# Optimization experiments

Hardware: AMD Instinct MI355X
Metric: run time of the kernel (lower is better)

The kernel has to match this reference:

```python
import jax, jax.numpy as jnp
import numpy as np

B, T, D_IN = 2048, 26, 512
H = 512          # hidden_size
E = 256          # num_char_embeddings
C = 97           # num_class
S = 32           # num_steps = batch_max_length + 1


def setup_inputs() -> dict:
    key = jax.random.key(0)
    ks = jax.random.split(key, 16)
    sc = lambda n: 1.0 / np.sqrt(n)
    inp = {
        "batch_H": jax.random.normal(ks[0], (B, T, D_IN), jnp.float32),
        "text": jax.random.randint(ks[1], (B, S), 0, C),
        # attention cell params
        "W_i2h": jax.random.normal(ks[2], (H, D_IN), jnp.float32) * sc(D_IN),
        "W_h2h": jax.random.normal(ks[3], (H, H), jnp.float32) * sc(H),
        "b_h2h": jax.random.normal(ks[4], (H,), jnp.float32) * sc(H),
        "w_score": jax.random.normal(ks[5], (1, H), jnp.float32) * sc(H),
        # LSTMCell params (gate order: i, f, g, o)
        "W_ih": jax.random.normal(ks[6], (4 * H, D_IN + E), jnp.float32) * sc(D_IN + E),
        "W_hh": jax.random.normal(ks[7], (4 * H, H), jnp.float32) * sc(H),
        "b_ih": jax.random.normal(ks[8], (4 * H,), jnp.float32) * sc(H),
        "b_hh": jax.random.normal(ks[9], (4 * H,), jnp.float32) * sc(H),
        # generator + char embedding
        "W_gen": jax.random.normal(ks[10], (C, H), jnp.float32) * sc(H),
        "b_gen": jax.random.normal(ks[11], (C,), jnp.float32) * sc(H),
        "emb_table": jax.random.normal(ks[12], (C, E), jnp.float32),
    }
    return inp


def _decode(batch_H, text, W_i2h, W_h2h, b_h2h, w_score,
            W_ih, W_hh, b_ih, b_hh, emb_table):
    # i2h(batch_H) is constant across steps -> hoist out of the loop
    Hp = jnp.einsum('btd,hd->bth', batch_H, W_i2h)          # [B,T,H]
    char_embs = emb_table[text]                              # [B,S,E]
    h0 = jnp.zeros((batch_H.shape[0], H), batch_H.dtype)
    c0 = jnp.zeros_like(h0)

    def step(carry, ce):
        h, c = carry
        ph = h @ W_h2h.T + b_h2h                             # [B,H]
        e = jnp.tanh(Hp + ph[:, None, :]) @ w_score[0]       # [B,T]
        alpha = jax.nn.softmax(e, axis=1)                    # [B,T]
        context = jnp.einsum('bt,btd->bd', alpha, batch_H)   # [B,D_IN]
        x = jnp.concatenate([context, ce], axis=1)           # [B,D_IN+E]
        gates = x @ W_ih.T + b_ih + h @ W_hh.T + b_hh        # [B,4H]
        i, f, g, o = jnp.split(gates, 4, axis=1)
        c_new = jax.nn.sigmoid(f) * c + jax.nn.sigmoid(i) * jnp.tanh(g)
        h_new = jax.nn.sigmoid(o) * jnp.tanh(c_new)
        return (h_new, c_new), h_new

    _, hs = jax.lax.scan(step, (h0, c0), jnp.swapaxes(char_embs, 0, 1))
    return jnp.swapaxes(hs, 0, 1)                            # [B,S,H]


def reference(batch_H, text, W_i2h, W_h2h, b_h2h, w_score,
              W_ih, W_hh, b_ih, b_hh, W_gen, b_gen, emb_table):
    output_hiddens = _decode(batch_H, text, W_i2h, W_h2h, b_h2h, w_score,
                             W_ih, W_hh, b_ih, b_hh, emb_table)
    probs = output_hiddens @ W_gen.T + b_gen                 # [B,S,C]
    return probs
```

## Files before the change

### kernel.cpp

```cpp
#include <hip/hip_runtime.h>

#define BB 2048
#define TT 26
#define DIN 512
#define HH 512
#define EE 256
#define CC 97
#define SS 32
#define G4 2048
#define XK2 1024

typedef unsigned short u16;
typedef __bf16 bf16x8 __attribute__((ext_vector_type(8)));
typedef float f32x4 __attribute__((ext_vector_type(4)));

__device__ __forceinline__ float bf2f(u16 u) {
    return __uint_as_float(((unsigned int)u) << 16);
}
__device__ __forceinline__ u16 f2bf(float f) {
    unsigned int u = __float_as_uint(f);
    u = u + 0x7FFFu + ((u >> 16) & 1u);
    return (u16)(u >> 16);
}
__device__ __forceinline__ float th_f(float x) {
    return 1.0f - 2.0f * __builtin_amdgcn_rcpf(__expf(2.0f * x) + 1.0f);
}
__device__ __forceinline__ float sig_f(float x) {
    return __builtin_amdgcn_rcpf(1.0f + __expf(-x));
}

__device__ __forceinline__ void async16(const u16* g, u16* l) {
    __builtin_amdgcn_global_load_lds(
        (const __attribute__((address_space(1))) unsigned int*)(g),
        (__attribute__((address_space(3))) unsigned int*)(l), 16, 0, 0);
}

__global__ __launch_bounds__(256) void gemm128(
    const u16* __restrict__ A, int lda,
    const u16* __restrict__ W,
    u16* __restrict__ Cout, int ldc, int K)
{
    __shared__ __align__(16) u16 As[128 * 32];
    __shared__ __align__(16) u16 Ws[128 * 32];

    const int tid  = threadIdx.x;
    const int lane = tid & 63;
    const int wave = tid >> 6;
    const int m0 = blockIdx.y * 128;
    const int n0 = blockIdx.x * 128;

    const int srow = tid >> 2;
    const int scol = (tid & 3) * 8;
    const u16* Arow0 = A + (size_t)(m0 + srow) * lda + scol;
    const u16* Arow1 = A + (size_t)(m0 + 64 + srow) * lda + scol;
    const u16* Wrow0 = W + (size_t)(n0 + srow) * K + scol;
    const u16* Wrow1 = W + (size_t)(n0 + 64 + srow) * K + scol;
    u16* dstA0 = As + wave * 512;
    u16* dstA1 = As + 2048 + wave * 512;
    u16* dstW0 = Ws + wave * 512;
    u16* dstW1 = Ws + 2048 + wave * 512;

    const int wm = (wave >> 1) * 64;
    const int wn = (wave & 1) * 64;
    const int fr = lane & 15;
    const int fq = lane >> 4;

    f32x4 acc[4][4];
    #pragma unroll
    for (int i = 0; i < 4; i++)
        #pragma unroll
        for (int j = 0; j < 4; j++)
            #pragma unroll
            for (int r = 0; r < 4; r++) acc[i][j][r] = 0.0f;

    for (int k0 = 0; k0 < K; k0 += 32) {
        async16(Arow0 + k0, dstA0);
        async16(Arow1 + k0, dstA1);
        async16(Wrow0 + k0, dstW0);
        async16(Wrow1 + k0, dstW1);
        __syncthreads();
        bf16x8 af[4], bw[4];
        #pragma unroll
        for (int i = 0; i < 4; i++)
            af[i] = *(const bf16x8*)&As[(wm + i * 16 + fr) * 32 + fq * 8];
        #pragma unroll
        for (int j = 0; j < 4; j++)
            bw[j] = *(const bf16x8*)&Ws[(wn + j * 16 + fr) * 32 + fq * 8];
        #pragma unroll
        for (int i = 0; i < 4; i++)
            #pragma unroll
            for (int j = 0; j < 4; j++)
                acc[i][j] = __builtin_amdgcn_mfma_f32_16x16x32_bf16(
                    af[i], bw[j], acc[i][j], 0, 0, 0);
        __syncthreads();
    }

    #pragma unroll
    for (int j = 0; j < 4; j++) {
        int col = n0 + wn + j * 16 + fr;
        #pragma unroll
        for (int i = 0; i < 4; i++) {
            int row = m0 + wm + i * 16 + fq * 4;
            #pragma unroll
            for (int r = 0; r < 4; r++)
                Cout[(size_t)(row + r) * ldc + col] = f2bf(acc[i][j][r]);
        }
    }
}

__global__ __launch_bounds__(256) void gen128(
    const u16* __restrict__ A,
    const u16* __restrict__ Wg,
    const float* __restrict__ bgen,
    float* __restrict__ out)
{
    __shared__ __align__(16) u16 As[128 * 32];
    __shared__ __align__(16) u16 Ws[128 * 32];

    const int tid  = threadIdx.x;
    const int lane = tid & 63;
    const int wave = tid >> 6;
    const int m0 = blockIdx.y * 128;

    const int srow = tid >> 2;
    const int scol = (tid & 3) * 8;
    const u16* Arow0 = A + (size_t)(m0 + srow) * HH + scol;
    const u16* Arow1 = A + (size_t)(m0 + 64 + srow) * HH + scol;
    const u16* Wrow0 = Wg + (size_t)srow * HH + scol;
    const u16* Wrow1 = Wg + (size_t)(64 + srow) * HH + scol;
    u16* dstA0 = As + wave * 512;
    u16* dstA1 = As + 2048 + wave * 512;
    u16* dstW0 = Ws + wave * 512;
    u16* dstW1 = Ws + 2048 + wave * 512;

    const int wm = (wave >> 1) * 64;
    const int wn = (wave & 1) * 64;
    const int fr = lane & 15;
    const int fq = lane >> 4;

    f32x4 acc[4][4];
    #pragma unroll
    for (int i = 0; i < 4; i++)
        #pragma unroll
        for (int j = 0; j < 4; j++)
            #pragma unroll
            for (int r = 0; r < 4; r++) acc[i][j][r] = 0.0f;

    for (int k0 = 0; k0 < HH; k0 += 32) {
        async16(Arow0 + k0, dstA0);
        async16(Arow1 + k0, dstA1);
        async16(Wrow0 + k0, dstW0);
        async16(Wrow1 + k0, dstW1);
        __syncthreads();
        bf16x8 af[4], bw[4];
        #pragma unroll
        for (int i = 0; i < 4; i++)
            af[i] = *(const bf16x8*)&As[(wm + i * 16 + fr) * 32 + fq * 8];
        #pragma unroll
        for (int j = 0; j < 4; j++)
            bw[j] = *(const bf16x8*)&Ws[(wn + j * 16 + fr) * 32 + fq * 8];
        #pragma unroll
        for (int i = 0; i < 4; i++)
            #pragma unroll
            for (int j = 0; j < 4; j++)
                acc[i][j] = __builtin_amdgcn_mfma_f32_16x16x32_bf16(
                    af[i], bw[j], acc[i][j], 0, 0, 0);
        __syncthreads();
    }

    #pragma unroll
    for (int j = 0; j < 4; j++) {
        int col = wn + j * 16 + fr;
        if (col < CC) {
            float bv = bgen[col];
            #pragma unroll
            for (int i = 0; i < 4; i++) {
                int row = m0 + wm + i * 16 + fq * 4;
                #pragma unroll
                for (int r = 0; r < 4; r++) {
                    int m = row + r;
                    int s = m >> 11, b = m & (BB - 1);
                    out[(size_t)b * (SS * CC) + s * CC + col] = acc[i][j][r] + bv;
                }
            }
        }
    }
}

__global__ __launch_bounds__(256) void gates_lstm(
    const u16* __restrict__ ctx,
    const u16* __restrict__ hprev,
    const u16* __restrict__ Wc,
    const float* __restrict__ bcat,
    const float* __restrict__ P,
    const int* __restrict__ text,
    float* __restrict__ c,
    u16* __restrict__ hnext,
    int s)
{
    __shared__ __align__(16) u16 As[64 * 32];
    __shared__ __align__(16) u16 Ws[128 * 32];
    __shared__ float gsm[64 * 68];
    __shared__ int text_sm[64];

    const int tid  = threadIdx.x;
    const int lane = tid & 63;
    const int wave = tid >> 6;

    int b   = blockIdx.y * gridDim.x + blockIdx.x;
    int xcd = b & 7, loc = b >> 3;
    int by = (xcd & 3) * 8 + (loc & 7);
    int bx = (xcd >> 2) * 8 + (loc >> 3);
    const int m0 = by * 64;
    const int n0 = bx * 128;

    if (tid < 64) text_sm[tid] = text[(m0 + tid) * SS + s];

    const int srow = tid >> 2;
    const int scol = (tid & 3) * 8;
    const u16* Actx  = ctx   + (size_t)(m0 + srow) * 512 + scol;
    const u16* Ahid  = hprev + (size_t)(m0 + srow) * 512 + scol;
    const u16* Wrow0 = Wc + (size_t)(n0 + srow) * XK2 + scol;
    const u16* Wrow1 = Wc + (size_t)(n0 + 64 + srow) * XK2 + scol;
    u16* dstA  = As + wave * 512;
    u16* dstW0 = Ws + wave * 512;
    u16* dstW1 = Ws + 2048 + wave * 512;

    const int wm = (wave & 1) * 32;
    const int wn = (wave >> 1) * 64;
    const int fr = lane & 15;
    const int fq = lane >> 4;

    f32x4 acc[2][4];
    #pragma unroll
    for (int i = 0; i < 2; i++)
        #pragma unroll
        for (int j = 0; j < 4; j++)
            #pragma unroll
            for (int r = 0; r < 4; r++) acc[i][j][r] = 0.0f;

    #pragma unroll
    for (int k0 = 0; k0 < XK2; k0 += 32) {
        const u16* asrc = (k0 < 512) ? (Actx + k0) : (Ahid + (k0 - 512));
        async16(asrc, dstA);
        async16(Wrow0 + k0, dstW0);
        async16(Wrow1 + k0, dstW1);
        __syncthreads();
        bf16x8 af[2], bw[4];
        #pragma unroll
        for (int i = 0; i < 2; i++)
            af[i] = *(const bf16x8*)&As[(wm + i * 16 + fr) * 32 + fq * 8];
        #pragma unroll
        for (int j = 0; j < 4; j++)
            bw[j] = *(const bf16x8*)&Ws[(wn + j * 16 + fr) * 32 + fq * 8];
        #pragma unroll
        for (int i = 0; i < 2; i++)
            #pragma unroll
            for (int j = 0; j < 4; j++)
                acc[i][j] = __builtin_amdgcn_mfma_f32_16x16x32_bf16(
                    af[i], bw[j], acc[i][j], 0, 0, 0);
        __syncthreads();
    }

    #pragma unroll
    for (int p = 0; p < 2; p++) {
        if ((wave >> 1) == p) {
            #pragma unroll
            for (int j = 0; j < 4; j++) {
                int cl = j * 16 + fr;
                #pragma unroll
                for (int i = 0; i < 2; i++) {
                    int rl = wm + i * 16 + fq * 4;
                    #pragma unroll
                    for (int r = 0; r < 4; r++)
                        gsm[(rl + r) * 68 + cl] = acc[i][j][r];
                }
            }
        }
        __syncthreads();
        #pragma unroll
        for (int rr = 0; rr < 4; rr++) {
            int idx = rr * 256 + tid;
            int u = idx & 15, row = idx >> 4;
            int base = row * 68 + 4 * u;
            int hg = (n0 >> 2) + p * 16 + u;
            int c0 = 4 * hg;
            int ch = text_sm[row];
            float4 bc = *(const float4*)(bcat + c0);
            float4 pv = *(const float4*)(P + (size_t)ch * G4 + c0);
            float ig = sig_f(gsm[base]     + bc.x + pv.x);
            float fg = sig_f(gsm[base + 1] + bc.y + pv.y);
            float gg = th_f (gsm[base + 2] + bc.z + pv.z);
            float og = sig_f(gsm[base + 3] + bc.w + pv.w);
            size_t ci = (size_t)(m0 + row) * HH + hg;
            float cn = fg * c[ci] + ig * gg;
            c[ci] = cn;
            hnext[(size_t)(m0 + row) * HH + hg] = f2bf(og * th_f(cn));
        }
        __syncthreads();
    }
}

__global__ __launch_bounds__(256) void gemm64(
    const u16* __restrict__ A, int lda,
    const u16* __restrict__ W, int ldw,
    const float* __restrict__ bias,
    float* __restrict__ Cout, int ldc, int K, int use_bias)
{
    __shared__ __align__(16) u16 As[64][32];
    __shared__ __align__(16) u16 Ws[64][32];

    const int tid  = threadIdx.x;
    const int lane = tid & 63;
    const int wave = tid >> 6;
    const int m0 = blockIdx.y * 64;
    const int n0 = blockIdx.x * 64;
    const int ar = tid >> 2;
    const int ac = (tid & 3) * 8;
    const int wm = (wave >> 1) * 32;
    const int wn = (wave & 1) * 32;
    const int fr = lane & 15;
    const int fq = lane >> 4;

    f32x4 acc[2][2];
    #pragma unroll
    for (int i = 0; i < 2; i++)
        #pragma unroll
        for (int j = 0; j < 2; j++)
            #pragma unroll
            for (int r = 0; r < 4; r++) acc[i][j][r] = 0.0f;

    const u16* Arow = A + (size_t)(m0 + ar) * lda;
    const u16* Wrow = W + (size_t)(n0 + ar) * ldw;

    for (int k0 = 0; k0 < K; k0 += 32) {
        *(uint4*)&As[ar][ac] = *(const uint4*)(Arow + k0 + ac);
        *(uint4*)&Ws[ar][ac] = *(const uint4*)(Wrow + k0 + ac);
        __syncthreads();
        bf16x8 af[2], bw[2];
        #pragma unroll
        for (int mm = 0; mm < 2; mm++)
            af[mm] = *(const bf16x8*)&As[wm + mm * 16 + fr][fq * 8];
        #pragma unroll
        for (int nn = 0; nn < 2; nn++)
            bw[nn] = *(const bf16x8*)&Ws[wn + nn * 16 + fr][fq * 8];
        #pragma unroll
        for (int mm = 0; mm < 2; mm++)
            #pragma unroll
            for (int nn = 0; nn < 2; nn++)
                acc[mm][nn] = __builtin_amdgcn_mfma_f32_16x16x32_bf16(
                    af[mm], bw[nn], acc[mm][nn], 0, 0, 0);
        __syncthreads();
    }

    #pragma unroll
    for (int nn = 0; nn < 2; nn++) {
        int col = n0 + wn + nn * 16 + fr;
        float bv = use_bias ? bias[col] : 0.0f;
        #pragma unroll
        for (int mm = 0; mm < 2; mm++) {
            int row = m0 + wm + mm * 16 + fq * 4;
            #pragma unroll
            for (int r = 0; r < 4; r++)
                Cout[(size_t)(row + r) * ldc + col] = acc[mm][nn][r] + bv;
        }
    }
}

__global__ __launch_bounds__(256) void attn_step(
    const u16* __restrict__ Hp, const float* __restrict__ ph,
    const float* __restrict__ wscore, const u16* __restrict__ bH16,
    u16* __restrict__ ctx)
{
    const int b = blockIdx.x;
    const int tid = threadIdx.x, lane = tid & 63, wave = tid >> 6;
    __shared__ float e_sm[32];
    __shared__ float alpha_sm[32];

    const int h8 = lane * 8;
    float ph_r[8], ws_r[8];
    {
        float4 p0 = *(const float4*)(ph + (size_t)b * HH + h8);
        float4 p1 = *(const float4*)(ph + (size_t)b * HH + h8 + 4);
        ph_r[0]=p0.x; ph_r[1]=p0.y; ph_r[2]=p0.z; ph_r[3]=p0.w;
        ph_r[4]=p1.x; ph_r[5]=p1.y; ph_r[6]=p1.z; ph_r[7]=p1.w;
        float4 w0 = *(const float4*)(wscore + h8);
        float4 w1 = *(const float4*)(wscore + h8 + 4);
        ws_r[0]=w0.x; ws_r[1]=w0.y; ws_r[2]=w0.z; ws_r[3]=w0.w;
        ws_r[4]=w1.x; ws_r[5]=w1.y; ws_r[6]=w1.z; ws_r[7]=w1.w;
    }

    for (int t = wave; t < TT; t += 4) {
        uint4 hv = *(const uint4*)(Hp + ((size_t)b * TT + t) * HH + h8);
        const u16* hu = (const u16*)&hv;
        float sum = 0.0f;
        #pragma unroll
        for (int j = 0; j < 8; j++)
            sum += th_f(bf2f(hu[j]) + ph_r[j]) * ws_r[j];
        #pragma unroll
        for (int off = 32; off > 0; off >>= 1) sum += __shfl_down(sum, off);
        if (lane == 0) e_sm[t] = sum;
    }
    __syncthreads();

    if (tid == 0) {
        float mx = e_sm[0];
        for (int t = 1; t < TT; t++) mx = fmaxf(mx, e_sm[t]);
        float ssum = 0.0f;
        for (int t = 0; t < TT; t++) {
            float ev = __expf(e_sm[t] - mx);
            alpha_sm[t] = ev;
            ssum += ev;
        }
        float inv = 1.0f / ssum;
        for (int t = 0; t < TT; t++) alpha_sm[t] *= inv;
    }
    __syncthreads();

    {
        int d0 = tid * 2;
        float c0 = 0.0f, c1 = 0.0f;
        const u16* bb = bH16 + (size_t)b * TT * DIN + d0;
        #pragma unroll
        for (int t = 0; t < TT; t++) {
            unsigned int v = *(const unsigned int*)(bb + (size_t)t * DIN);
            float a = alpha_sm[t];
            c0 += a * bf2f((u16)(v & 0xffffu));
            c1 += a * bf2f((u16)(v >> 16));
        }
        unsigned int o = (unsigned int)f2bf(c0) | ((unsigned int)f2bf(c1) << 16);
        *(unsigned int*)(ctx + (size_t)b * 512 + d0) = o;
    }
}

__global__ __launch_bounds__(256) void cast_f32_bf16(
    const float* __restrict__ src, u16* __restrict__ dst, int n)
{
    int i = (blockIdx.x * 256 + threadIdx.x) * 4;
    if (i < n) {
        float4 v = *(const float4*)(src + i);
        ushort4 o;
        o.x = f2bf(v.x); o.y = f2bf(v.y); o.z = f2bf(v.z); o.w = f2bf(v.w);
        *(ushort4*)(dst + i) = o;
    }
}

__global__ __launch_bounds__(256) void prep_all(
    const float* __restrict__ W_ih, const float* __restrict__ W_hh,
    const float* __restrict__ b_ih, const float* __restrict__ b_hh,
    const float* __restrict__ b_h2h, const float* __restrict__ emb,
    const float* __restrict__ W_i2h, const float* __restrict__ W_h2h,
    const float* __restrict__ W_gen,
    u16* __restrict__ Wcat, u16* __restrict__ Wce16, u16* __restrict__ emb16,
    u16* __restrict__ Wgen16, u16* __restrict__ Wi2h16, u16* __restrict__ Wh2h16,
    float* __restrict__ bcat, float* __restrict__ cst, u16* __restrict__ hid0,
    float* __restrict__ ph)
{
    int i = blockIdx.x * 256 + threadIdx.x;

    {
        int np = i >> 10, k = i & (XK2 - 1);
        int h = np >> 2, g = np & 3;
        int n = g * HH + h;
        float v = (k < 512) ? W_ih[(size_t)n * (DIN + EE) + k]
                            : W_hh[(size_t)n * HH + (k - 512)];
        Wcat[(size_t)i] = f2bf(v);
    }
    if (i < G4 * EE) {
        int np = i >> 8, e = i & (EE - 1);
        int h = np >> 2, g = np & 3;
        int n = g * HH + h;
        Wce16[i] = f2bf(W_ih[(size_t)n * (DIN + EE) + DIN + e]);
    }
    if (i < 128 * EE) {
        int ch = i >> 8, e = i & (EE - 1);
        emb16[i] = (ch < CC) ? f2bf(emb[(size_t)ch * EE + e]) : (u16)0;
    }
    if (i < 128 * HH) {
        int n = i >> 9, k = i & (HH - 1);
        Wgen16[i] = (n < CC) ? f2bf(W_gen[(size_t)n * HH + k]) : (u16)0;
    }
    if (i < HH * DIN) Wi2h16[i] = f2bf(W_i2h[i]);
    if (i < HH * HH)  Wh2h16[i] = f2bf(W_h2h[i]);
    if (i < G4) {
        int h = i >> 2, g = i & 3;
        int n = g * HH + h;
        bcat[i] = b_ih[n] + b_hh[n];
    }
    if (i < BB * HH) {
        cst[i] = 0.0f;
        hid0[i] = 0;
        ph[i] = b_h2h[i & (HH - 1)];
    }
}

#define BH16_OFF  ((size_t)0)
#define HP_OFF    ((size_t)54525952)
#define HID_OFF   ((size_t)109051904)
#define CTX_OFF   ((size_t)178257920)
#define WCAT_OFF  ((size_t)180355072)
#define WCE_OFF   ((size_t)184549376)
#define EMB16_OFF ((size_t)185597952)
#define WGEN_OFF  ((size_t)185663488)
#define WI2H_OFF  ((size_t)185794560)
#define WH2H_OFF  ((size_t)186318848)
#define BCAT_OFF  ((size_t)186843136)
#define P_OFF     ((size_t)186851328)
#define PH_OFF    ((size_t)187899904)
#define CST_OFF   ((size_t)192094208)

extern "C" void kernel_launch(void* const* d_in, const int* in_sizes, int n_in,
                              void* d_out, int out_size, void* d_ws, size_t ws_size,
                              hipStream_t stream)
{
    const float* batch_H = (const float*)d_in[0];
    const int*   text    = (const int*)d_in[1];
    const float* W_i2h   = (const float*)d_in[2];
    const float* W_h2h   = (const float*)d_in[3];
    const float* b_h2h   = (const float*)d_in[4];
    const float* w_score = (const float*)d_in[5];
    const float* W_ih    = (const float*)d_in[6];
    const float* W_hh    = (const float*)d_in[7];
    const float* b_ih    = (const float*)d_in[8];
    const float* b_hh    = (const float*)d_in[9];
    const float* W_gen   = (const float*)d_in[10];
    const float* b_gen   = (const float*)d_in[11];
    const float* emb     = (const float*)d_in[12];

    char* ws = (char*)d_ws;
    u16*   bH16   = (u16*)(ws + BH16_OFF);
    u16*   Hp     = (u16*)(ws + HP_OFF);
    u16*   hid    = (u16*)(ws + HID_OFF);
    u16*   ctx    = (u16*)(ws + CTX_OFF);
    u16*   Wcat   = (u16*)(ws + WCAT_OFF);
    u16*   Wce16  = (u16*)(ws + WCE_OFF);
    u16*   emb16  = (u16*)(ws + EMB16_OFF);
    u16*   Wgen16 = (u16*)(ws + WGEN_OFF);
    u16*   Wi2h16 = (u16*)(ws + WI2H_OFF);
    u16*   Wh2h16 = (u16*)(ws + WH2H_OFF);
    float* bcat   = (float*)(ws + BCAT_OFF);
    float* P      = (float*)(ws + P_OFF);
    float* ph     = (float*)(ws + PH_OFF);
    float* cst    = (float*)(ws + CST_OFF);
    float* out    = (float*)d_out;

    cast_f32_bf16<<<dim3((BB * TT * DIN / 4 + 255) / 256), 256, 0, stream>>>(
        batch_H, bH16, BB * TT * DIN);
    prep_all<<<dim3((G4 * XK2) / 256), 256, 0, stream>>>(
        W_ih, W_hh, b_ih, b_hh, b_h2h, emb, W_i2h, W_h2h, W_gen,
        Wcat, Wce16, emb16, Wgen16, Wi2h16, Wh2h16, bcat, cst, hid, ph);
    gemm64<<<dim3(G4 / 64, 128 / 64), 256, 0, stream>>>(
        emb16, EE, Wce16, EE, nullptr, P, G4, EE, 0);

    gemm128<<<dim3(HH / 128, (BB * TT) / 128), 256, 0, stream>>>(
        bH16, DIN, Wi2h16, Hp, HH, DIN);

    for (int s = 0; s < SS; s++) {
        u16* hprev = hid + (size_t)s * BB * HH;
        u16* hnext = hid + (size_t)(s + 1) * BB * HH;

        attn_step<<<dim3(BB), 256, 0, stream>>>(Hp, ph, w_score, bH16, ctx);

        gates_lstm<<<dim3(G4 / 128, BB / 64), 256, 0, stream>>>(
            ctx, hprev, Wcat, bcat, P, text, cst, hnext, s);

        gemm64<<<dim3(HH / 64, BB / 64), 256, 0, stream>>>(
            hnext, HH, Wh2h16, HH, b_h2h, ph, HH, HH, 1);
    }

    gen128<<<dim3(1, (SS * BB) / 128), 256, 0, stream>>>(
        hid + (size_t)BB * HH, Wgen16, b_gen, out);
}
```

Before: 1.810 ms.

## Fuse h2h projection into attention kernel with pre-swizzled MFMA weights

```diff
diff --git a/kernel.cpp b/kernel.cpp
--- a/kernel.cpp
+++ b/kernel.cpp
@@ -367,69 +367,129 @@
     }
 }
 
-__global__ __launch_bounds__(256) void attn_step(
-    const u16* __restrict__ Hp, const float* __restrict__ ph,
-    const float* __restrict__ wscore, const u16* __restrict__ bH16,
+__global__ __launch_bounds__(512) void attnph(
+    const u16* __restrict__ hprev,
+    const u16* __restrict__ Wsw,
+    const float* __restrict__ bh2h,
+    const u16* __restrict__ Hp,
+    const u16* __restrict__ bH16,
+    const float* __restrict__ wscore,
     u16* __restrict__ ctx)
 {
-    const int b = blockIdx.x;
-    const int tid = threadIdx.x, lane = tid & 63, wave = tid >> 6;
-    __shared__ float e_sm[32];
-    __shared__ float alpha_sm[32];
-
-    const int h8 = lane * 8;
-    float ph_r[8], ws_r[8];
+    __shared__ __align__(16) u16 As[16 * 512];
+    __shared__ __align__(16) float phs[8 * 512];
+    __shared__ float e_sm[8][28];
+    __shared__ float alpha_sm[8][28];
+
+    const int tid  = threadIdx.x;
+    const int lane = tid & 63;
+    const int wave = tid >> 6;
+    const int m0   = blockIdx.x * 8;
+    const int fr   = lane & 15;
+    const int fq   = lane >> 4;
+
     {
-        float4 p0 = *(const float4*)(ph + (size_t)b * HH + h8);
-        float4 p1 = *(const float4*)(ph + (size_t)b * HH + h8 + 4);
-        ph_r[0]=p0.x; ph_r[1]=p0.y; ph_r[2]=p0.z; ph_r[3]=p0.w;
-        ph_r[4]=p1.x; ph_r[5]=p1.y; ph_r[6]=p1.z; ph_r[7]=p1.w;
+        int row = tid >> 6;
+        int c0  = (tid & 63) * 8;
+        int sw  = (row & 7) << 4;
+        int b1  = (row * 1024 + c0 * 2) ^ sw;
+        int b2  = ((row + 8) * 1024 + c0 * 2) ^ sw;
+        *(uint4*)((char*)As + b1) =
+            *(const uint4*)(hprev + (size_t)(m0 + row) * 512 + c0);
+        uint4 z = make_uint4(0u, 0u, 0u, 0u);
+        *(uint4*)((char*)As + b2) = z;
+    }
+    __syncthreads();
+
+    f32x4 acc[4];
+    #pragma unroll
+    for (int j = 0; j < 4; j++)
+        #pragma unroll
+        for (int r = 0; r < 4; r++) acc[j][r] = 0.0f;
+
+    #pragma unroll
+    for (int kk = 0; kk < 16; kk++) {
+        int rb = (fr * 1024 + kk * 64 + fq * 16) ^ ((fr & 7) << 4);
+        bf16x8 af = *(const bf16x8*)((const char*)As + rb);
+        #pragma unroll
+        for (int j = 0; j < 4; j++) {
+            int jj = wave * 4 + j;
+            bf16x8 wv = *(const bf16x8*)&Wsw[((size_t)(jj * 16 + kk) * 64 + lane) * 8];
+            acc[j] = __builtin_amdgcn_mfma_f32_16x16x32_bf16(af, wv, acc[j], 0, 0, 0);
+        }
+    }
+    if (fq < 2) {
+        #pragma unroll
+        for (int j = 0; j < 4; j++) {
+            int n = wave * 64 + j * 16 + fr;
+            float bv = bh2h[n];
+            #pragma unroll
+            for (int r = 0; r < 4; r++)
+                phs[(fq * 4 + r) * 512 + n] = acc[j][r] + bv;
+        }
+    }
+    __syncthreads();
+
+    const int row = wave;
+    const int h8  = lane * 8;
+    float ws_r[8], ph_r[8];
+    {
         float4 w0 = *(const float4*)(wscore + h8);
         float4 w1 = *(const float4*)(wscore + h8 + 4);
         ws_r[0]=w0.x; ws_r[1]=w0.y; ws_r[2]=w0.z; ws_r[3]=w0.w;
         ws_r[4]=w1.x; ws_r[5]=w1.y; ws_r[6]=w1.z; ws_r[7]=w1.w;
-    }
-
-    for (int t = wave; t < TT; t += 4) {
-        uint4 hv = *(const uint4*)(Hp + ((size_t)b * TT + t) * HH + h8);
-        const u16* hu = (const u16*)&hv;
-        float sum = 0.0f;
-        #pragma unroll
-        for (int j = 0; j < 8; j++)
-            sum += th_f(bf2f(hu[j]) + ph_r[j]) * ws_r[j];
-        #pragma unroll
-        for (int off = 32; off > 0; off >>= 1) sum += __shfl_down(sum, off);
-        if (lane == 0) e_sm[t] = sum;
+        float4 p0 = *(const float4*)&phs[row * 512 + h8];
+        float4 p1 = *(const float4*)&phs[row * 512 + h8 + 4];
+        ph_r[0]=p0.x; ph_r[1]=p0.y; ph_r[2]=p0.z; ph_r[3]=p0.w;
+        ph_r[4]=p1.x; ph_r[5]=p1.y; ph_r[6]=p1.z; ph_r[7]=p1.w;
+    }
+    {
+        const u16* hpb = Hp + (size_t)(m0 + row) * TT * 512 + h8;
+        for (int t = 0; t < TT; t++) {
+            uint4 hv = *(const uint4*)(hpb + (size_t)t * 512);
+            const u16* hu = (const u16*)&hv;
+            float sum = 0.0f;
+            #pragma unroll
+            for (int j = 0; j < 8; j++)
+                sum += th_f(bf2f(hu[j]) + ph_r[j]) * ws_r[j];
+            #pragma unroll
+            for (int off = 32; off > 0; off >>= 1) sum += __shfl_down(sum, off);
+            if (lane == 0) e_sm[row][t] = sum;
+        }
     }
     __syncthreads();
 
-    if (tid == 0) {
-        float mx = e_sm[0];
-        for (int t = 1; t < TT; t++) mx = fmaxf(mx, e_sm[t]);
-        float ssum = 0.0f;
+    {
+        float ev = (lane < TT) ? e_sm[row][lane] : -3.0e38f;
+        float mx = ev;
+        #pragma unroll
+        for (int off = 32; off > 0; off >>= 1)
+            mx = fmaxf(mx, __shfl_xor(mx, off));
+        float p = (lane < TT) ? __expf(ev - mx) : 0.0f;
+        float ssum = p;
+        #pragma unroll
+        for (int off = 32; off > 0; off >>= 1) ssum += __shfl_xor(ssum, off);
+        if (lane < TT) alpha_sm[row][lane] = p / ssum;
+    }
+    __syncthreads();
+
+    {
+        float ca[8];
+        #pragma unroll
+        for (int j = 0; j < 8; j++) ca[j] = 0.0f;
+        const u16* bb = bH16 + (size_t)(m0 + row) * TT * 512 + h8;
+        #pragma unroll
         for (int t = 0; t < TT; t++) {
-            float ev = __expf(e_sm[t] - mx);
-            alpha_sm[t] = ev;
-            ssum += ev;
-        }
-        float inv = 1.0f / ssum;
-        for (int t = 0; t < TT; t++) alpha_sm[t] *= inv;
-    }
-    __syncthreads();
-
-    {
-        int d0 = tid * 2;
-        float c0 = 0.0f, c1 = 0.0f;
-        const u16* bb = bH16 + (size_t)b * TT * DIN + d0;
-        #pragma unroll
-        for (int t = 0; t < TT; t++) {
-            unsigned int v = *(const unsigned int*)(bb + (size_t)t * DIN);
-            float a = alpha_sm[t];
-            c0 += a * bf2f((u16)(v & 0xffffu));
-            c1 += a * bf2f((u16)(v >> 16));
-        }
-        unsigned int o = (unsigned int)f2bf(c0) | ((unsigned int)f2bf(c1) << 16);
-        *(unsigned int*)(ctx + (size_t)b * 512 + d0) = o;
+            uint4 v = *(const uint4*)(bb + (size_t)t * 512);
+            const u16* vu = (const u16*)&v;
+            float a = alpha_sm[row][t];
+            #pragma unroll
+            for (int j = 0; j < 8; j++) ca[j] += a * bf2f(vu[j]);
+        }
+        u16 o[8];
+        #pragma unroll
+        for (int j = 0; j < 8; j++) o[j] = f2bf(ca[j]);
+        *(uint4*)(ctx + (size_t)(m0 + row) * 512 + h8) = *(const uint4*)o;
     }
 }
 
@@ -448,13 +508,12 @@
 __global__ __launch_bounds__(256) void prep_all(
     const float* __restrict__ W_ih, const float* __restrict__ W_hh,
     const float* __restrict__ b_ih, const float* __restrict__ b_hh,
-    const float* __restrict__ b_h2h, const float* __restrict__ emb,
+    const float* __restrict__ emb,
     const float* __restrict__ W_i2h, const float* __restrict__ W_h2h,
     const float* __restrict__ W_gen,
     u16* __restrict__ Wcat, u16* __restrict__ Wce16, u16* __restrict__ emb16,
-    u16* __restrict__ Wgen16, u16* __restrict__ Wi2h16, u16* __restrict__ Wh2h16,
-    float* __restrict__ bcat, float* __restrict__ cst, u16* __restrict__ hid0,
-    float* __restrict__ ph)
+    u16* __restrict__ Wgen16, u16* __restrict__ Wi2h16, u16* __restrict__ Wsw,
+    float* __restrict__ bcat, float* __restrict__ cst, u16* __restrict__ hid0)
 {
     int i = blockIdx.x * 256 + threadIdx.x;
 
@@ -481,7 +540,12 @@
         Wgen16[i] = (n < CC) ? f2bf(W_gen[(size_t)n * HH + k]) : (u16)0;
     }
     if (i < HH * DIN) Wi2h16[i] = f2bf(W_i2h[i]);
-    if (i < HH * HH)  Wh2h16[i] = f2bf(W_h2h[i]);
+    if (i < HH * HH) {
+        int e = i & 7, l = (i >> 3) & 63, kk = (i >> 9) & 15, jj = i >> 13;
+        int rrow = jj * 16 + (l & 15);
+        int rcol = kk * 32 + (l >> 4) * 8 + e;
+        Wsw[i] = f2bf(W_h2h[(size_t)rrow * HH + rcol]);
+    }
     if (i < G4) {
         int h = i >> 2, g = i & 3;
         int n = g * HH + h;
@@ -490,7 +554,6 @@
     if (i < BB * HH) {
         cst[i] = 0.0f;
         hid0[i] = 0;
-        ph[i] = b_h2h[i & (HH - 1)];
     }
 }
 
@@ -503,10 +566,9 @@
 #define EMB16_OFF ((size_t)185597952)
 #define WGEN_OFF  ((size_t)185663488)
 #define WI2H_OFF  ((size_t)185794560)
-#define WH2H_OFF  ((size_t)186318848)
+#define WSW_OFF   ((size_t)186318848)
 #define BCAT_OFF  ((size_t)186843136)
 #define P_OFF     ((size_t)186851328)
-#define PH_OFF    ((size_t)187899904)
 #define CST_OFF   ((size_t)192094208)
 
 extern "C" void kernel_launch(void* const* d_in, const int* in_sizes, int n_in,
@@ -537,18 +599,17 @@
     u16*   emb16  = (u16*)(ws + EMB16_OFF);
     u16*   Wgen16 = (u16*)(ws + WGEN_OFF);
     u16*   Wi2h16 = (u16*)(ws + WI2H_OFF);
-    u16*   Wh2h16 = (u16*)(ws + WH2H_OFF);
+    u16*   Wsw    = (u16*)(ws + WSW_OFF);
     float* bcat   = (float*)(ws + BCAT_OFF);
     float* P      = (float*)(ws + P_OFF);
-    float* ph     = (float*)(ws + PH_OFF);
     float* cst    = (float*)(ws + CST_OFF);
     float* out    = (float*)d_out;
 
     cast_f32_bf16<<<dim3((BB * TT * DIN / 4 + 255) / 256), 256, 0, stream>>>(
         batch_H, bH16, BB * TT * DIN);
     prep_all<<<dim3((G4 * XK2) / 256), 256, 0, stream>>>(
-        W_ih, W_hh, b_ih, b_hh, b_h2h, emb, W_i2h, W_h2h, W_gen,
-        Wcat, Wce16, emb16, Wgen16, Wi2h16, Wh2h16, bcat, cst, hid, ph);
+        W_ih, W_hh, b_ih, b_hh, emb, W_i2h, W_h2h, W_gen,
+        Wcat, Wce16, emb16, Wgen16, Wi2h16, Wsw, bcat, cst, hid);
     gemm64<<<dim3(G4 / 64, 128 / 64), 256, 0, stream>>>(
         emb16, EE, Wce16, EE, nullptr, P, G4, EE, 0);
 
@@ -559,13 +620,11 @@
         u16* hprev = hid + (size_t)s * BB * HH;
         u16* hnext = hid + (size_t)(s + 1) * BB * HH;
 
-        attn_step<<<dim3(BB), 256, 0, stream>>>(Hp, ph, w_score, bH16, ctx);
+        attnph<<<dim3(BB / 8), 512, 0, stream>>>(
+            hprev, Wsw, b_h2h, Hp, bH16, w_score, ctx);
 
         gates_lstm<<<dim3(G4 / 128, BB / 64), 256, 0, stream>>>(
             ctx, hprev, Wcat, bcat, P, text, cst, hnext, s);
-
-        gemm64<<<dim3(HH / 64, BB / 64), 256, 0, stream>>>(
-            hnext, HH, Wh2h16, HH, b_h2h, ph, HH, HH, 1);
     }
 
     gen128<<<dim3(1, (SS * BB) / 128), 256, 0, stream>>>(
```

Result: slower. 2.043 ms (+12.8%).
